# Optimization experiments

Measured on AMD Instinct MI355X. Metric: run time of the kernel, lower is better.

The kernel has to match this reference:

```python
import jax, jax.numpy as jnp
import numpy as np

WINDOW = 512
STEP = WINDOW // 2


def hamming_window(n):
    # torch.hamming_window default is periodic=True: 0.54 - 0.46*cos(2*pi*k/n)
    return (0.54 - 0.46 * jnp.cos(2.0 * jnp.pi * jnp.arange(n) / n)).astype(jnp.float32)


def fft_convolve(a, b):
    # ortho-normalized rfft spectra, irfft, crop back to n samples.
    n = a.shape[-1]
    pa = jnp.pad(a, [(0, 0)] * (a.ndim - 1) + [(0, n)])
    pb = jnp.pad(b, [(0, 0)] * (b.ndim - 1) + [(0, n)])
    spec = jnp.fft.rfft(pa, axis=-1, norm='ortho') * jnp.fft.rfft(pb, axis=-1, norm='ortho')
    return jnp.fft.irfft(spec, n=2 * n, axis=-1, norm='ortho')[..., :n]


def fft_shift(a, shift):
    # repo's fft_shift: fractional shift via phase ramp in rfft domain of the
    n = a.shape[-1]
    shift_samples = shift * n * 0.5  # [..., 1]
    pa = jnp.pad(a, [(0, 0)] * (a.ndim - 1) + [(0, n)])
    spec = jnp.fft.rfft(pa, axis=-1, norm='ortho')  # [..., n+1]
    n_coeffs = spec.shape[-1]
    ramp = (jnp.arange(n_coeffs) * 2j * jnp.pi) / n_coeffs
    phase = jnp.exp(-ramp * shift_samples)  # broadcast over last dim
    return jnp.fft.irfft(spec * phase, n=2 * n, axis=-1, norm='ortho')


def setup_inputs() -> dict:
    key = jax.random.key(0)
    k1, k2 = jax.random.split(key)
    B, n = 4, 32768
    recon = jax.random.normal(k1, (B, 1, n), dtype=jnp.float32)
    target = jax.random.normal(k2, (B, 1, n), dtype=jnp.float32)
    return {"recon": recon, "target": target}


def reference(recon, target):
    batch = recon.shape[0]
    n_samples = recon.shape[-1]
    n_frames = (n_samples - WINDOW) // STEP + 1  # unfold(-1, 512, 256)

    # unfold: gather overlapping frames [B, n_frames, WINDOW]
    idx = jnp.arange(n_frames)[:, None] * STEP + jnp.arange(WINDOW)[None, :]
    frames = recon[:, 0, :][:, idx]  # [B, n_frames, WINDOW]
    windowed = (frames * hamming_window(WINDOW))[:, None, :, :]  # [B,1,F,W]

    # zero-pad each frame up to n_samples (the torch.cat with zeros)
    windowed = jnp.pad(windowed, ((0, 0), (0, 0), (0, 0), (0, n_samples - WINDOW)))

    # FFT cross-correlation surrogate against the full target
    fm = fft_convolve(windowed, target[:, :, None, :])[..., :n_samples]  # [B,1,F,n]

    positions = jnp.argmax(fm, axis=-1, keepdims=True).astype(jnp.float32) / n_samples

    positioned = fft_shift(windowed, positions)[..., :n_samples]  # [B,1,F,n]
    positioned = jnp.sum(positioned, axis=2).reshape(batch, 1, n_samples)

    return jnp.mean((positioned - target) ** 2)
```

## Files before the change

kernel.cpp:

```cpp
#include <hip/hip_runtime.h>
#include <math.h>

#define N_SAMP   32768
#define WINDOW   512
#define STEP     256
#define NFRAMES  127
#define NB       4
#define RTRUNC   1280
#define NSLAB    32
#define BPAD     776
#define HW       3104
#define VSTRIDE  193

#define WS_WF   0
#define WS_WFH  260096
#define WS_WFL  391168
#define WS_PV   522240
#define WS_M    587776
#define WS_CNT  588288
#define WS_LIST 588304
#define WS_H    592400
#define WS_PART 2169232

typedef _Float16 f16x8 __attribute__((ext_vector_type(8)));
typedef float f32x16 __attribute__((ext_vector_type(16)));

#define SW(L) ((L) ^ (((L) >> 3) & 7))

#define FMA4(A, LO, HI)                                           \
    A.x = fmaf(c.x, HI.x, A.x); A.x = fmaf(c.y, LO.w, A.x);       \
    A.x = fmaf(c.z, LO.z, A.x); A.x = fmaf(c.w, LO.y, A.x);       \
    A.y = fmaf(c.x, HI.y, A.y); A.y = fmaf(c.y, HI.x, A.y);       \
    A.y = fmaf(c.z, LO.w, A.y); A.y = fmaf(c.w, LO.z, A.y);       \
    A.z = fmaf(c.x, HI.z, A.z); A.z = fmaf(c.y, HI.y, A.z);       \
    A.z = fmaf(c.z, HI.x, A.z); A.z = fmaf(c.w, LO.w, A.z);       \
    A.w = fmaf(c.x, HI.w, A.w); A.w = fmaf(c.y, HI.z, A.w);       \
    A.w = fmaf(c.z, HI.y, A.w); A.w = fmaf(c.w, HI.x, A.w);

__global__ __launch_bounds__(256) void k_wf(const float* __restrict__ recon,
                                            float* __restrict__ wf,
                                            _Float16* __restrict__ wfh,
                                            float* __restrict__ part,
                                            int nslab) {
    int e = blockIdx.x * 256 + threadIdx.x;
    int w     = e & 511;
    int bf128 = e >> 9;
    int f = bf128 & 127;
    int b = bf128 >> 7;
    float val = 0.f;
    if (f < NFRAMES) {
        float ham = 0.54f - 0.46f * (float)cos((double)w * (M_PI / 256.0));
        val = ham * recon[b * N_SAMP + f * STEP + w];
        wf[(b * NFRAMES + f) * 512 + w] = val;
    }
    size_t tr = (((size_t)b * 64 + (w >> 3)) * 128 + f) * 8 + (w & 7);
    wfh[tr] = (_Float16)val;
    float4* p4 = (float4*)part;
    int nq = nslab * 32768;
    for (int q = e; q < nq; q += 262144)
        p4[q] = make_float4(0.f, 0.f, 0.f, 0.f);
}

__global__ __launch_bounds__(256, 4) void k_argmax_mfma(
        const float* __restrict__ tgt,
        const _Float16* __restrict__ wfh,
        float* __restrict__ pv) {
    __shared__ _Float16 sbh[8 * BPAD];
    __shared__ __align__(16) float stf[768];
    const int tid   = threadIdx.x;
    const int chunk = blockIdx.x & 127;
    const int half  = (blockIdx.x >> 7) & 1;
    const int b     = blockIdx.x >> 8;
    const int T0    = chunk * 256;
    const int TB    = T0 + 255;
    const float* tb = tgt + b * N_SAMP;

    if (tid < 192) {
        int A = TB - 767 + 4 * tid;
        float4 vq = (A >= 0) ? *(const float4*)(tb + A)
                             : make_float4(0.f, 0.f, 0.f, 0.f);
        *(float4*)(stf + 4 * tid) = vq;
    }
    __syncthreads();
    for (int oc = tid; oc < 768; oc += 256) {
        int r = oc / 96, s = oc - r * 96;
        int y0 = 767 - r - 8 * s;
        _Float16 h8[8];
#pragma unroll
        for (int j = 0; j < 8; ++j)
            h8[j] = (_Float16)stf[y0 - j];
        *(f16x8*)&sbh[r * BPAD + 8 * s] = *(f16x8*)h8;
    }
    __syncthreads();

    const int wv  = tid >> 6;
    const int q   = (tid >> 5) & 1;
    const int cl  = tid & 31;
    const int nt0 = 2 * wv;
    const int rp  = 7 - (cl & 7);
    const _Float16* Ah0 = wfh + ((size_t)b * 64) * 1024 + (half * 64 + cl) * 8;

    f32x16 acc00 = (f32x16)(0.f);
    f32x16 acc01 = (f32x16)(0.f);
    f32x16 acc10 = (f32x16)(0.f);
    f32x16 acc11 = (f32x16)(0.f);

    int off = q * 1024;
    int ea  = rp * BPAD + (255 - 32 * nt0 - cl + 8 * q - rp);
    f16x8 a0  = *(const f16x8*)(Ah0 + off);
    f16x8 a1  = *(const f16x8*)(Ah0 + off + 256);
    f16x8 bh0 = *(const f16x8*)&sbh[ea];
    f16x8 bh1 = *(const f16x8*)&sbh[ea - 32];
#pragma unroll
    for (int k0 = 0; k0 < 512; k0 += 16) {
        f16x8 a0n  = *(const f16x8*)(Ah0 + off + 2048);
        f16x8 a1n  = *(const f16x8*)(Ah0 + off + 2304);
        f16x8 bh0n = *(const f16x8*)&sbh[ea + 16];
        f16x8 bh1n = *(const f16x8*)&sbh[ea - 16];
        acc00 = __builtin_amdgcn_mfma_f32_32x32x16_f16(a0, bh0, acc00, 0, 0, 0);
        acc01 = __builtin_amdgcn_mfma_f32_32x32x16_f16(a0, bh1, acc01, 0, 0, 0);
        acc10 = __builtin_amdgcn_mfma_f32_32x32x16_f16(a1, bh0, acc10, 0, 0, 0);
        acc11 = __builtin_amdgcn_mfma_f32_32x32x16_f16(a1, bh1, acc11, 0, 0, 0);
        a0 = a0n; a1 = a1n; bh0 = bh0n; bh1 = bh1n;
        off += 2048; ea += 16;
    }

    __syncthreads();
    float* sval = (float*)sbh;
#pragma unroll
    for (int r = 0; r < 16; ++r) {
        float v0 = fmaxf(acc00[r], acc01[r]);
        float v1 = fmaxf(acc10[r], acc11[r]);
#pragma unroll
        for (int mm = 1; mm <= 16; mm <<= 1) {
            v0 = fmaxf(v0, __shfl_xor(v0, mm));
            v1 = fmaxf(v1, __shfl_xor(v1, mm));
        }
        if (cl == 0) {
            int row = (r & 3) + 8 * (r >> 2) + 4 * q;
            sval[row * 4 + wv]        = v0;
            sval[(32 + row) * 4 + wv] = v1;
        }
    }
    __syncthreads();
    if (tid < 64) {
        float v = fmaxf(fmaxf(sval[tid * 4], sval[tid * 4 + 1]),
                        fmaxf(sval[tid * 4 + 2], sval[tid * 4 + 3]));
        pv[((size_t)b * 128 + half * 64 + tid) * 128 + chunk] = v;
    }
}

__global__ __launch_bounds__(256) void k_vmax(const float* __restrict__ tgt,
                                              const float* __restrict__ wf,
                                              const float* __restrict__ pv,
                                              int* __restrict__ marr) {
    __shared__ __align__(16) float stg[4 * VSTRIDE * 4];
    __shared__ float rv[256];
    __shared__ int   ri[256];
    __shared__ int   clist[32];
    __shared__ int   ccnt;
    const int tid  = threadIdx.x;
    const int lane = tid & 63;
    const int wv   = tid >> 6;
    const int fr   = blockIdx.x;
    const int b    = fr / NFRAMES;
    const int f    = fr - b * NFRAMES;
    const float* prow = pv + ((size_t)b * 128 + f) * 128;
    const float* tb   = tgt + b * N_SAMP;
    const float4* wcg = (const float4*)(wf + (size_t)fr * 512);

    float mv = (tid < 128) ? prow[tid] : -3.4e38f;
    rv[tid] = mv;
    __syncthreads();
    for (int s = 128; s > 0; s >>= 1) {
        if (tid < s) rv[tid] = fmaxf(rv[tid], rv[tid + s]);
        __syncthreads();
    }
    float m0 = rv[0];
    if (tid == 0) ccnt = 0;
    __syncthreads();
    float eps = 0.012f * fabsf(m0) + 1e-3f;
    if (tid < 128 && mv >= m0 - eps) {
        int k = atomicAdd(&ccnt, 1);
        if (k < 32) clist[k] = tid;
    }
    __syncthreads();
    int nc = ccnt;
    int total = (nc <= 32) ? nc : 128;
    float bestv = -3.4e38f; int bestt = 0x7fffffff;
    float* myg = stg + wv * (VSTRIDE * 4);

    for (int ci = wv; ci < total; ci += 4) {
        int c2 = (nc <= 32) ? clist[ci] : ci;
        int T0 = c2 * 256;
        for (int e = lane; e < 192; e += 64) {
            int A = T0 - 512 + 4 * e;
            float4 vq = (A >= 0 && A < N_SAMP) ? *(const float4*)(tb + A)
                                               : make_float4(0.f, 0.f, 0.f, 0.f);
            *(float4*)(myg + 4 * e) = vq;
        }
        float4 acc = make_float4(0.f, 0.f, 0.f, 0.f);
        float4 lo = *(const float4*)(myg + 4 * (lane + 127));
        float4 hi = *(const float4*)(myg + 4 * (lane + 128));
        for (int g = 0; g < 127; ++g) {
            float4 nl = *(const float4*)(myg + 4 * (lane + 126 - g));
            const float4 c = wcg[g];
            FMA4(acc, lo, hi);
            hi = lo; lo = nl;
        }
        {
            const float4 c = wcg[127];
            FMA4(acc, lo, hi);
        }
        int tt = T0 + 4 * lane;
        if (acc.x > bestv || (acc.x == bestv && tt     < bestt)) { bestv = acc.x; bestt = tt;     }
        if (acc.y > bestv || (acc.y == bestv && tt + 1 < bestt)) { bestv = acc.y; bestt = tt + 1; }
        if (acc.z > bestv || (acc.z == bestv && tt + 2 < bestt)) { bestv = acc.z; bestt = tt + 2; }
        if (acc.w > bestv || (acc.w == bestv && tt + 3 < bestt)) { bestv = acc.w; bestt = tt + 3; }
    }
    rv[tid] = bestv; ri[tid] = bestt;
    __syncthreads();
    for (int s = 128; s > 0; s >>= 1) {
        if (tid < s) {
            float v2 = rv[tid + s]; int i2 = ri[tid + s];
            if (v2 > rv[tid] || (v2 == rv[tid] && i2 < ri[tid])) {
                rv[tid] = v2; ri[tid] = i2;
            }
        }
        __syncthreads();
    }
    if (tid == 0) marr[fr] = ri[0];
}

__global__ __launch_bounds__(256) void k_coef(const int* __restrict__ marr,
                                              float* __restrict__ hbuf,
                                              int* __restrict__ list,
                                              int* __restrict__ cnt,
                                              int nslab,
                                              float* __restrict__ out) {
    const int tid = threadIdx.x;

    if (blockIdx.x == NB * NFRAMES) {
        __shared__ int scnt[64];
        __shared__ int total;
        if (tid == 0) out[0] = 0.0f;
        if (tid < 64) scnt[tid] = 0;
        if (tid == 0) total = 0;
        __syncthreads();
        const int RT8 = RTRUNC + 8;
        for (int bf = tid; bf < NB * NFRAMES; bf += 256) {
            int b = bf / NFRAMES;
            int m = marr[bf];
            int p = (int)rint((double)m * (32768.0 / 32769.0));
            int lo = p - RT8;        if (lo < 0) lo = 0;
            int hi = p + RT8 + 511;  if (hi > N_SAMP - 1) hi = N_SAMP - 1;
            int r0 = lo >> 11, r1 = hi >> 11;
            for (int r = r0; r <= r1; ++r) {
                int bc = (b << 4) | r;
                int s = atomicAdd(&scnt[bc], 1);
                int k = atomicAdd(&total, 1);
                list[k] = (bf << 16) | (r << 8) | s;
            }
        }
        __syncthreads();
        int n = total;
        for (int k = tid; k < n; k += 256) {
            int v = list[k];
            int bf = (v >> 16) & 0x3fff;
            int r = (v >> 8) & 15;
            int b = bf / NFRAMES;
            if (scnt[(b << 4) | r] > nslab) list[k] = v | (1 << 30);
        }
        if (tid == 0) {
            int mx = 0;
            for (int i = 0; i < 64; ++i) mx = (scnt[i] > mx) ? scnt[i] : mx;
            cnt[0] = n;
            cnt[1] = (mx > nslab) ? nslab : mx;
        }
        return;
    }

    const int bf  = blockIdx.x;
    const double invD = 1.0 / 2147549184.0;
    const float  sd   = 4.7936899603827e-05f;
    const float  trf  = (float)(RTRUNC + 4) / 65536.0f;
    int m = marr[bf];
    int p = (int)rint((double)m * (32768.0 / 32769.0));
    int jlo = p - (RTRUNC + 8); if (jlo < -512) jlo = -512; jlo &= ~3;
    float* hr = hbuf + (size_t)bf * HW;
    if (m == 0) {
        for (int k4 = tid; k4 < 776; k4 += 256) {
            int j0 = jlo + 4 * k4;
            float4 vq = make_float4((j0 == 0) ? 1.0f : 0.0f, 0.f, 0.f, 0.f);
            *(float4*)(hr + 4 * k4) = vq;
        }
        return;
    }
    double md32768 = (double)m * 32768.0;
    double sp = sin((double)m * (M_PI / 32769.0));
    float Cp = (float)(sp * (1.0 / 65536.0));
    if (m & 1) Cp = -Cp;
    float Cn = -Cp;
    for (int k4 = tid; k4 < 776; k4 += 256) {
        int j0 = jlo + 4 * k4;
        double A0 = (double)j0 * 32769.0 - md32768;
        double rA0 = A0 * invD;
        float f0v = (float)(rA0 - rint(rA0));
        float4 vq;
        if (fabsf(f0v) > trf) {
            vq = make_float4(0.f, 0.f, 0.f, 0.f);
        } else if (fabsf(f0v) < 6.2e-5f) {
#pragma unroll
            for (int k = 0; k < 4; ++k) {
                double rA = (A0 + (double)k * 32769.0) * invD;
                float ff = (float)(rA - rint(rA));
                float r2;
                if (ff == 0.0f) r2 = 65535.0f;
                else {
                    float s, c2;
                    __sincosf((float)M_PI * ff, &s, &c2);
                    r2 = c2 * __builtin_amdgcn_rcpf(s);
                }
                ((float*)&vq)[k] = ((k & 1) ? Cn : Cp) * r2;
            }
        } else {
            float s, c2;
            __sincosf((float)M_PI * f0v, &s, &c2);
            vq.x = Cp * (c2 * __builtin_amdgcn_rcpf(s));
            float s1 = fmaf(c2, sd, s);
            float c1 = fmaf(-s, sd, c2);
            vq.y = Cn * (c1 * __builtin_amdgcn_rcpf(s1));
            float s2 = fmaf(c1, sd, s1);
            float cc2 = fmaf(-s1, sd, c1);
            vq.z = Cp * (cc2 * __builtin_amdgcn_rcpf(s2));
            float s3 = fmaf(cc2, sd, s2);
            float c3 = fmaf(-s2, sd, cc2);
            vq.w = Cn * (c3 * __builtin_amdgcn_rcpf(s3));
        }
        *(float4*)(hr + 4 * k4) = vq;
    }
}

#define LDBLK2(nn) (*(const float4*)(s_h + 4 * SW(Lt + (nn))))
#define CB3(g, A, Bq, Cq)                                         \
    {                                                             \
        float4 tnew = LDBLK2(126 - (g));                          \
        const float4 c = wc[(g)];                                 \
        FMA4(acc0, w[A], w[Bq]); FMA4(acc1, w[Bq], w[Cq]);        \
        w[Cq] = tnew;                                             \
    }
#define CB3_NL(g, A, Bq, Cq)                                      \
    {                                                             \
        const float4 c = wc[(g)];                                 \
        FMA4(acc0, w[A], w[Bq]); FMA4(acc1, w[Bq], w[Cq]);        \
    }

__global__ __launch_bounds__(256, 8) void k_shift_acc(const float* __restrict__ wf,
                                                      const int* __restrict__ marr,
                                                      const int* __restrict__ list,
                                                      const int* __restrict__ cnt,
                                                      const float* __restrict__ hbuf,
                                                      float* __restrict__ part,
                                                      int slabmask) {
    __shared__ __align__(16) float s_h[2560];
    const int tid = threadIdx.x;
    const int Lt  = 2 * tid;
    const int Ltw = (tid >> 6) * 128;
    const int n   = cnt[0];

    for (int se = blockIdx.x; se < n; se += gridDim.x) {
        int v     = list[se];
        int bf    = (v >> 16) & 0x3fff;
        int r     = (v >> 8) & 15;
        int slot  = v & 255;
        int isat  = (v >> 30) & 1;
        int b     = bf / NFRAMES;
        int t0s   = r << 11;
        const float4* __restrict__ wc = (const float4*)(wf + bf * 512);

        int m  = marr[bf];
        int pr = (int)rint((double)m * (32768.0 / 32769.0));
        int jlo = pr - (RTRUNC + 8); if (jlo < -512) jlo = -512; jlo &= ~3;
        int kb0 = ((t0s - 512) - jlo) >> 2;
        const float4* __restrict__ hb = (const float4*)(hbuf + (size_t)bf * HW);

        __syncthreads();
        for (int e4 = tid; e4 < 640; e4 += 256) {
            int kb = kb0 + e4;
            float4 vq = (kb >= 0 && kb < 776) ? hb[kb]
                                              : make_float4(0.f, 0.f, 0.f, 0.f);
            *(float4*)(s_h + 4 * SW(e4)) = vq;
        }
        __syncthreads();

        int blo = (pr - (RTRUNC + 8) - (t0s - 512)) >> 2;
        int bhi = (pr + (RTRUNC + 8) - (t0s - 512)) >> 2;
        if (blo < 0) blo = 0;
        if (bhi > 639) bhi = 639;

        float4 acc0 = make_float4(0.f, 0.f, 0.f, 0.f);
        float4 acc1 = acc0;

        int gmin = Ltw + 127 - bhi; if (gmin < 0) gmin = 0;
        int gmax = Ltw + 255 - blo; if (gmax > 127) gmax = 127;
        if (gmin <= gmax) {
            int go0 = gmin / 3;
            bool tail = (gmax >= 126);
            int goE = tail ? 42 : (gmax / 3 + 1);
            int gb0 = 3 * go0;
            float4 w[3];
            w[0] = LDBLK2(127 - gb0);
            w[1] = LDBLK2(128 - gb0);
            w[2] = LDBLK2(129 - gb0);
            for (int go = go0; go < goE && go < 42; ++go) {
                const int gb = 3 * go;
                CB3(gb + 0, 0, 1, 2);
                CB3(gb + 1, 2, 0, 1);
                CB3(gb + 2, 1, 2, 0);
            }
            if (tail) { CB3(126, 0, 1, 2); CB3_NL(127, 2, 0, 1); }
        }

        int slab = slot & slabmask;
        float* ob = part + (size_t)slab * (NB * N_SAMP) + b * N_SAMP + t0s;
        if (!isat) {
            *(float4*)(ob + 8 * tid)     = acc0;
            *(float4*)(ob + 8 * tid + 4) = acc1;
        } else {
            float* p0 = ob + 8 * tid;
            atomicAdd(p0 + 0, acc0.x); atomicAdd(p0 + 1, acc0.y);
            atomicAdd(p0 + 2, acc0.z); atomicAdd(p0 + 3, acc0.w);
            atomicAdd(p0 + 4, acc1.x); atomicAdd(p0 + 5, acc1.y);
            atomicAdd(p0 + 6, acc1.z); atomicAdd(p0 + 7, acc1.w);
        }
    }
}

__global__ __launch_bounds__(256) void k_mse(const float* __restrict__ part,
                                             const float* __restrict__ tgt,
                                             float* __restrict__ out,
                                             const int* __restrict__ cnt,
                                             int nslab) {
    __shared__ float sred[4];
    int e = blockIdx.x * 256 + threadIdx.x;
    int ng = cnt[1];
    if (ng > nslab) ng = nslab;
    float s0 = 0.f, s1 = 0.f, s2 = 0.f, s3 = 0.f;
    int g = 0;
    for (; g + 4 <= ng; g += 4) {
        s0 += part[(size_t)(g + 0) * (NB * N_SAMP) + e];
        s1 += part[(size_t)(g + 1) * (NB * N_SAMP) + e];
        s2 += part[(size_t)(g + 2) * (NB * N_SAMP) + e];
        s3 += part[(size_t)(g + 3) * (NB * N_SAMP) + e];
    }
    for (; g < ng; ++g)
        s0 += part[(size_t)g * (NB * N_SAMP) + e];
    float s = (s0 + s1) + (s2 + s3);
    float d = s - tgt[e];
    float v = d * d;
#pragma unroll
    for (int off = 32; off > 0; off >>= 1) v += __shfl_down(v, off, 64);
    int lane = threadIdx.x & 63, wid = threadIdx.x >> 6;
    if (lane == 0) sred[wid] = v;
    __syncthreads();
    if (threadIdx.x == 0) {
        float sm = sred[0] + sred[1] + sred[2] + sred[3];
        atomicAdd(out, sm * (1.0f / 131072.0f));
    }
}

extern "C" void kernel_launch(void* const* d_in, const int* in_sizes, int n_in,
                              void* d_out, int out_size, void* d_ws, size_t ws_size,
                              hipStream_t stream) {
    const float* recon = (const float*)d_in[0];
    const float* tgt   = (const float*)d_in[1];
    float* out = (float*)d_out;
    float* W   = (float*)d_ws;

    float*     wf   = W + WS_WF;
    _Float16*  wfh  = (_Float16*)(W + WS_WFH);
    float*     pv   = W + WS_PV;
    int*       marr = (int*)(W + WS_M);
    int*       cnt  = (int*)(W + WS_CNT);
    int*       list = (int*)(W + WS_LIST);
    float*     hbuf = W + WS_H;
    float*     part = W + WS_PART;

    int nslab = NSLAB;
    while (nslab > 1 &&
           ((size_t)WS_PART + (size_t)nslab * NB * N_SAMP) * sizeof(float) > ws_size)
        nslab >>= 1;

    k_wf<<<1024, 256, 0, stream>>>(recon, wf, wfh, part, nslab);
    k_argmax_mfma<<<1024, 256, 0, stream>>>(tgt, wfh, pv);
    k_vmax<<<NB * NFRAMES, 256, 0, stream>>>(tgt, wf, pv, marr);
    k_coef<<<NB * NFRAMES + 1, 256, 0, stream>>>(marr, hbuf, list, cnt, nslab, out);
    k_shift_acc<<<2048, 256, 0, stream>>>(wf, marr, list, cnt, hbuf, part, nslab - 1);
    k_mse<<<512, 256, 0, stream>>>(part, tgt, out, cnt, nslab);
}
```

Measured before the change: 157.2 us.

## Fuse coefficient generation into vmax kernel and rewrite shift loop with 5-way rotation

```diff
diff --git a/kernel.cpp b/kernel.cpp
--- a/kernel.cpp
+++ b/kernel.cpp
@@ -150,10 +150,11 @@
     }
 }
 
-__global__ __launch_bounds__(256) void k_vmax(const float* __restrict__ tgt,
-                                              const float* __restrict__ wf,
-                                              const float* __restrict__ pv,
-                                              int* __restrict__ marr) {
+__global__ __launch_bounds__(256) void k_vmax_coef(const float* __restrict__ tgt,
+                                                   const float* __restrict__ wf,
+                                                   const float* __restrict__ pv,
+                                                   int* __restrict__ marr,
+                                                   float* __restrict__ hbuf) {
     __shared__ __align__(16) float stg[4 * VSTRIDE * 4];
     __shared__ float rv[256];
     __shared__ int   ri[256];
@@ -229,65 +230,15 @@
         }
         __syncthreads();
     }
-    if (tid == 0) marr[fr] = ri[0];
-}
-
-__global__ __launch_bounds__(256) void k_coef(const int* __restrict__ marr,
-                                              float* __restrict__ hbuf,
-                                              int* __restrict__ list,
-                                              int* __restrict__ cnt,
-                                              int nslab,
-                                              float* __restrict__ out) {
-    const int tid = threadIdx.x;
-
-    if (blockIdx.x == NB * NFRAMES) {
-        __shared__ int scnt[64];
-        __shared__ int total;
-        if (tid == 0) out[0] = 0.0f;
-        if (tid < 64) scnt[tid] = 0;
-        if (tid == 0) total = 0;
-        __syncthreads();
-        const int RT8 = RTRUNC + 8;
-        for (int bf = tid; bf < NB * NFRAMES; bf += 256) {
-            int b = bf / NFRAMES;
-            int m = marr[bf];
-            int p = (int)rint((double)m * (32768.0 / 32769.0));
-            int lo = p - RT8;        if (lo < 0) lo = 0;
-            int hi = p + RT8 + 511;  if (hi > N_SAMP - 1) hi = N_SAMP - 1;
-            int r0 = lo >> 11, r1 = hi >> 11;
-            for (int r = r0; r <= r1; ++r) {
-                int bc = (b << 4) | r;
-                int s = atomicAdd(&scnt[bc], 1);
-                int k = atomicAdd(&total, 1);
-                list[k] = (bf << 16) | (r << 8) | s;
-            }
-        }
-        __syncthreads();
-        int n = total;
-        for (int k = tid; k < n; k += 256) {
-            int v = list[k];
-            int bf = (v >> 16) & 0x3fff;
-            int r = (v >> 8) & 15;
-            int b = bf / NFRAMES;
-            if (scnt[(b << 4) | r] > nslab) list[k] = v | (1 << 30);
-        }
-        if (tid == 0) {
-            int mx = 0;
-            for (int i = 0; i < 64; ++i) mx = (scnt[i] > mx) ? scnt[i] : mx;
-            cnt[0] = n;
-            cnt[1] = (mx > nslab) ? nslab : mx;
-        }
-        return;
-    }
-
-    const int bf  = blockIdx.x;
+    int m = ri[0];
+    if (tid == 0) marr[fr] = m;
+
     const double invD = 1.0 / 2147549184.0;
     const float  sd   = 4.7936899603827e-05f;
     const float  trf  = (float)(RTRUNC + 4) / 65536.0f;
-    int m = marr[bf];
     int p = (int)rint((double)m * (32768.0 / 32769.0));
     int jlo = p - (RTRUNC + 8); if (jlo < -512) jlo = -512; jlo &= ~3;
-    float* hr = hbuf + (size_t)bf * HW;
+    float* hr = hbuf + (size_t)fr * HW;
     if (m == 0) {
         for (int k4 = tid; k4 < 776; k4 += 256) {
             int j0 = jlo + 4 * k4;
@@ -341,19 +292,51 @@
     }
 }
 
-#define LDBLK2(nn) (*(const float4*)(s_h + 4 * SW(Lt + (nn))))
-#define CB3(g, A, Bq, Cq)                                         \
-    {                                                             \
-        float4 tnew = LDBLK2(126 - (g));                          \
-        const float4 c = wc[(g)];                                 \
-        FMA4(acc0, w[A], w[Bq]); FMA4(acc1, w[Bq], w[Cq]);        \
-        w[Cq] = tnew;                                             \
-    }
-#define CB3_NL(g, A, Bq, Cq)                                      \
-    {                                                             \
-        const float4 c = wc[(g)];                                 \
-        FMA4(acc0, w[A], w[Bq]); FMA4(acc1, w[Bq], w[Cq]);        \
-    }
+__global__ __launch_bounds__(256) void k_sched(const int* __restrict__ marr,
+                                               int* __restrict__ list,
+                                               int* __restrict__ cnt,
+                                               int nslab,
+                                               float* __restrict__ out) {
+    __shared__ int scnt[64];
+    __shared__ int total;
+    const int tid = threadIdx.x;
+    if (tid == 0) out[0] = 0.0f;
+    if (tid < 64) scnt[tid] = 0;
+    if (tid == 0) total = 0;
+    __syncthreads();
+    const int RT8 = RTRUNC + 8;
+    for (int bf = tid; bf < NB * NFRAMES; bf += 256) {
+        int b = bf / NFRAMES;
+        int m = marr[bf];
+        int p = (int)rint((double)m * (32768.0 / 32769.0));
+        int lo = p - RT8;        if (lo < 0) lo = 0;
+        int hi = p + RT8 + 511;  if (hi > N_SAMP - 1) hi = N_SAMP - 1;
+        int r0 = lo >> 11, r1 = hi >> 11;
+        for (int r = r0; r <= r1; ++r) {
+            int bc = (b << 4) | r;
+            int s = atomicAdd(&scnt[bc], 1);
+            int k = atomicAdd(&total, 1);
+            list[k] = (bf << 16) | (r << 8) | s;
+        }
+    }
+    __syncthreads();
+    int n = total;
+    for (int k = tid; k < n; k += 256) {
+        int v = list[k];
+        int bf = (v >> 16) & 0x3fff;
+        int r = (v >> 8) & 15;
+        int b = bf / NFRAMES;
+        if (scnt[(b << 4) | r] > nslab) list[k] = v | (1 << 30);
+    }
+    if (tid == 0) {
+        int mx = 0;
+        for (int i = 0; i < 64; ++i) mx = (scnt[i] > mx) ? scnt[i] : mx;
+        cnt[0] = n;
+        cnt[1] = (mx > nslab) ? nslab : mx;
+    }
+}
+
+#define LDB(nn) (*(const float4*)(s_h + 4 * SW(nn)))
 
 __global__ __launch_bounds__(256, 8) void k_shift_acc(const float* __restrict__ wf,
                                                       const int* __restrict__ marr,
@@ -404,21 +387,37 @@
         int gmin = Ltw + 127 - bhi; if (gmin < 0) gmin = 0;
         int gmax = Ltw + 255 - blo; if (gmax > 127) gmax = 127;
         if (gmin <= gmax) {
-            int go0 = gmin / 3;
-            bool tail = (gmax >= 126);
-            int goE = tail ? 42 : (gmax / 3 + 1);
-            int gb0 = 3 * go0;
-            float4 w[3];
-            w[0] = LDBLK2(127 - gb0);
-            w[1] = LDBLK2(128 - gb0);
-            w[2] = LDBLK2(129 - gb0);
-            for (int go = go0; go < goE && go < 42; ++go) {
-                const int gb = 3 * go;
-                CB3(gb + 0, 0, 1, 2);
-                CB3(gb + 1, 2, 0, 1);
-                CB3(gb + 2, 1, 2, 0);
+            int gb0 = (gmin / 5) * 5;
+            float4 s1v = LDB(Lt + 126 - gb0);
+            float4 s2v = LDB(Lt + 127 - gb0);
+            float4 s3v = LDB(Lt + 128 - gb0);
+            float4 s4v = LDB(Lt + 129 - gb0);
+            float4 s0v = s1v;
+            int gend = (gmax < 120) ? gmax : 120;
+            for (int gb = gb0; gb <= gend; gb += 5) {
+                float4 t0 = LDB(Lt + 125 - gb);
+                { const float4 c = wc[gb];     FMA4(acc0, s2v, s3v); FMA4(acc1, s3v, s4v); }
+                s0v = t0;
+                float4 t1 = LDB(Lt + 124 - gb);
+                { const float4 c = wc[gb + 1]; FMA4(acc0, s1v, s2v); FMA4(acc1, s2v, s3v); }
+                s4v = t1;
+                float4 t2 = LDB(Lt + 123 - gb);
+                { const float4 c = wc[gb + 2]; FMA4(acc0, s0v, s1v); FMA4(acc1, s1v, s2v); }
+                s3v = t2;
+                float4 t3 = LDB(Lt + 122 - gb);
+                { const float4 c = wc[gb + 3]; FMA4(acc0, s4v, s0v); FMA4(acc1, s0v, s1v); }
+                s2v = t3;
+                float4 t4 = LDB(Lt + 121 - gb);
+                { const float4 c = wc[gb + 4]; FMA4(acc0, s3v, s4v); FMA4(acc1, s4v, s0v); }
+                s1v = t4;
             }
-            if (tail) { CB3(126, 0, 1, 2); CB3_NL(127, 2, 0, 1); }
+            if (gmax >= 125) {
+                float4 t0 = LDB(Lt);
+                { const float4 c = wc[125]; FMA4(acc0, s2v, s3v); FMA4(acc1, s3v, s4v); }
+                s0v = t0;
+                { const float4 c = wc[126]; FMA4(acc0, s1v, s2v); FMA4(acc1, s2v, s3v); }
+                { const float4 c = wc[127]; FMA4(acc0, s0v, s1v); FMA4(acc1, s1v, s2v); }
+            }
         }
 
         int slab = slot & slabmask;
@@ -493,8 +492,8 @@
 
     k_wf<<<1024, 256, 0, stream>>>(recon, wf, wfh, part, nslab);
     k_argmax_mfma<<<1024, 256, 0, stream>>>(tgt, wfh, pv);
-    k_vmax<<<NB * NFRAMES, 256, 0, stream>>>(tgt, wf, pv, marr);
-    k_coef<<<NB * NFRAMES + 1, 256, 0, stream>>>(marr, hbuf, list, cnt, nslab, out);
+    k_vmax_coef<<<NB * NFRAMES, 256, 0, stream>>>(tgt, wf, pv, marr, hbuf);
+    k_sched<<<1, 256, 0, stream>>>(marr, list, cnt, nslab, out);
     k_shift_acc<<<2048, 256, 0, stream>>>(wf, marr, list, cnt, hbuf, part, nslab - 1);
     k_mse<<<512, 256, 0, stream>>>(part, tgt, out, cnt, nslab);
 }
```

New measurement: 154.5 us. About the same (-1.7%).
